# Kernel tuning notes

Measured on AMD Instinct MI355X. Metric: run time of the kernel, lower is better.

Reference implementation:

```python
import jax, jax.numpy as jnp
from jax import lax
import numpy as np

N_MTF = 41

def _gaussian2d(N, std):
    t = np.arange(-(N - 1) / 2, (N + 1) / 2)
    t1, t2 = np.meshgrid(t, t)
    return np.exp(-0.5 * (t1 / std) ** 2) * np.exp(-0.5 * (t2 / std) ** 2)

def _kaiser2d(N, beta):
    t = np.arange(-(N - 1) / 2, (N + 1) / 2) / np.double(N - 1)
    t1, t2 = np.meshgrid(t, t)
    t12 = np.sqrt(t1 * t1 + t2 * t2)
    w1 = np.kaiser(N, beta)
    w = np.interp(t12, t, w1)
    w[t12 > t[-1]] = 0
    w[t12 < t[0]] = 0
    return w

def _fir_filter_wind(Hd, w):
    hd = np.rot90(np.fft.fftshift(np.rot90(Hd, 2)), 2)
    h = np.fft.fftshift(np.fft.ifft2(hd))
    h = np.rot90(h, 2)
    return h * w

def gen_mtf_kernels(ratio, nbands):
    GNyq = np.asarray([0.34, 0.32, 0.3, 0.22], dtype='float32')[:nbands]  # QB sensor
    h = np.zeros((nbands, N_MTF, N_MTF), dtype='float32')
    fcut = 1.0 / ratio
    for ii in range(nbands):
        alpha = np.sqrt(((N_MTF - 1) * (fcut / 2)) ** 2 / (-2 * np.log(GNyq[ii])))
        H = _gaussian2d(N_MTF, alpha)
        Hd = H / np.max(H)
        w = _kaiser2d(N_MTF, 0.5)
        h[ii] = np.real(_fir_filter_wind(Hd, w)).astype('float32')
    return h

def gen_interp23_kernel():
    cdf23 = 2.0 * np.array([0.5, 0.305334091185, 0.0, -0.072698593239, 0.0,
                            0.021809577942, 0.0, -0.005192756653, 0.0,
                            0.000807762146, 0.0, -6.0081482e-05])
    d = cdf23[::-1]
    return np.concatenate([d[:-1], cdf23]).astype('float32')  # 23 taps

_DN = ('NCHW', 'OIHW', 'NCHW')

def _sep_filter_circular(img, k):
    # img: (bs, c, H, W); k: (K,) separable kernel, circular padding per torch F.pad('circular')
    bs, c, H, W = img.shape
    P = (k.shape[0] - 1) // 2
    f = img.reshape(bs * c, 1, H, W)
    f = jnp.pad(f, ((0, 0), (0, 0), (0, 0), (P, P)), mode='wrap')
    f = lax.conv_general_dilated(f, k.reshape(1, 1, 1, -1), (1, 1), 'VALID', dimension_numbers=_DN)
    f = jnp.pad(f, ((0, 0), (0, 0), (P, P), (0, 0)), mode='wrap')
    f = lax.conv_general_dilated(f, k.reshape(1, 1, -1, 1), (1, 1), 'VALID', dimension_numbers=_DN)
    return f.reshape(bs, c, H, W)

def interp23tap(x, kernel, num_upsamples):
    cur = x
    for k in range(num_upsamples):
        bs, c, h, w = cur.shape
        up = jnp.zeros((bs, c, 2 * h, 2 * w), cur.dtype)
        if k == 0:
            up = up.at[..., 1::2, 1::2].set(cur)
        else:
            up = up.at[..., ::2, ::2].set(cur)
        cur = _sep_filter_circular(up, kernel)
    return cur

def setup_inputs() -> dict:
    key = jax.random.key(0)
    bs, nbands, H, W = 4, 4, 1024, 1024
    ratio = 4
    x = jax.random.normal(key, (bs, nbands, H, W), dtype=jnp.float32)
    mtf_kernels = jnp.asarray(gen_mtf_kernels(ratio, nbands))          # (nbands, 41, 41)
    interp_kernel = jnp.asarray(gen_interp23_kernel())                  # (23,)
    pan_weights = jnp.full((nbands,), 1.0 / nbands, dtype=jnp.float32)  # 'mean' pan weights
    return {"x": x, "mtf_kernels": mtf_kernels, "interp_kernel": interp_kernel,
            "pan_weights": pan_weights, "ratio": ratio}

def reference(x, mtf_kernels, interp_kernel, pan_weights, ratio):
    # Simulated PAN: spectral weighting of HR bands
    pan = jnp.einsum('bchw,c->bhw', x, pan_weights)[:, None]  # (bs,1,H,W)
    # MTF blur: depthwise 41x41 conv with replicate padding
    nbands = x.shape[1]
    pad = mtf_kernels.shape[-1] // 2
    xp = jnp.pad(x, ((0, 0), (0, 0), (pad, pad), (pad, pad)), mode='edge')
    blurred = lax.conv_general_dilated(xp, mtf_kernels[:, None], (1, 1), 'VALID',
                                       dimension_numbers=_DN, feature_group_count=nbands)
    # Downsample: avgpool with kernel=stride=ratio
    bs, c, H, W = blurred.shape
    lrms = blurred.reshape(bs, c, H // ratio, ratio, W // ratio, ratio).mean(axis=(3, 5))
    # Upsample back via 23-tap polynomial interpolation (ratio = 2**num_upsamples)
    num_ups = int(ratio).bit_length() - 1
    ms_up = interp23tap(lrms, interp_kernel, num_ups)
    return pan, lrms, ms_up
```

## Files before the change

kernel.cpp:

```cpp
#include <hip/hip_runtime.h>

#define PAN_SZ  4194304
#define LRMS_OFF 4194304
#define MS_OFF  5242880

__global__ __launch_bounds__(256) void build_keff_kernel(
    const float* __restrict__ mtf, float* __restrict__ keff) {
  int e = blockIdx.x * 256 + threadIdx.x;
  if (e >= 4 * 44 * 44) return;
  int c = e / 1936;
  int rem = e - c * 1936;
  int p = rem / 44;
  int q = rem - p * 44;
  float s = 0.f;
  for (int di = 0; di < 4; ++di) {
    int u = p - di;
    if (u < 0 || u > 40) continue;
    for (int dj = 0; dj < 4; ++dj) {
      int v = q - dj;
      if (v < 0 || v > 40) continue;
      s += mtf[(c * 41 + u) * 41 + v];
    }
  }
  keff[e] = s * 0.0625f;
}

__global__ __launch_bounds__(256) void pan_kernel(
    const float* __restrict__ x, const float* __restrict__ w,
    float* __restrict__ pan) {
  int g = blockIdx.x * 256 + threadIdx.x;
  int b = g >> 18;
  int e = g & 262143;
  const float4* x4 = (const float4*)x;
  float w0 = w[0], w1 = w[1], w2 = w[2], w3 = w[3];
  float4 a0 = x4[(size_t)(b * 4 + 0) * 262144 + e];
  float4 a1 = x4[(size_t)(b * 4 + 1) * 262144 + e];
  float4 a2 = x4[(size_t)(b * 4 + 2) * 262144 + e];
  float4 a3 = x4[(size_t)(b * 4 + 3) * 262144 + e];
  float4 o;
  o.x = a0.x * w0 + a1.x * w1 + a2.x * w2 + a3.x * w3;
  o.y = a0.y * w0 + a1.y * w1 + a2.y * w2 + a3.y * w3;
  o.z = a0.z * w0 + a1.z * w1 + a2.z * w2 + a3.z * w3;
  o.w = a0.w * w0 + a1.w * w1 + a2.w * w2 + a3.w * w3;
  ((float4*)pan)[g] = o;
}

__global__ __launch_bounds__(256) void lrms_kernel(
    const float* __restrict__ x, const float* __restrict__ keff,
    float* __restrict__ lrms) {
  int img = blockIdx.y;
  int ch  = img & 3;
  int i0  = blockIdx.x * 8;
  int oc  = threadIdx.x;

  const float* ximg = x + (size_t)img * 1048576;
  const float* Kc   = keff + ch * 1936;

  float acc[8] = {0.f, 0.f, 0.f, 0.f, 0.f, 0.f, 0.f, 0.f};
  int c4base = oc - 5;
  bool interior = (oc >= 5) && (oc <= 250);

  float4 va[11], vb[11];

  auto loadrow = [&](int tt, float4* v) {
    int gy = 4 * i0 - 20 + tt;
    gy = gy < 0 ? 0 : (gy > 1023 ? 1023 : gy);
    const float4* row4 = (const float4*)(ximg + (size_t)gy * 1024);
    if (interior) {
      #pragma unroll
      for (int a = 0; a < 11; ++a) v[a] = row4[c4base + a];
    } else {
      const float* rowf = (const float*)row4;
      #pragma unroll
      for (int a = 0; a < 11; ++a) {
        int c4 = c4base + a;
        if ((unsigned)c4 <= 255u) {
          v[a] = row4[c4];
        } else {
          float4 t;
          t.x = rowf[min(max(4 * c4 + 0, 0), 1023)];
          t.y = rowf[min(max(4 * c4 + 1, 0), 1023)];
          t.z = rowf[min(max(4 * c4 + 2, 0), 1023)];
          t.w = rowf[min(max(4 * c4 + 3, 0), 1023)];
          v[a] = t;
        }
      }
    }
  };

  auto compute = [&](int tt, const float4* v) {
    #pragma unroll
    for (int r = 0; r < 8; ++r) {
      int p = tt - 4 * r;
      if ((unsigned)p < 44u) {
        const float* Kr = Kc + __builtin_amdgcn_readfirstlane(p * 44);
        float s = acc[r];
        #pragma unroll
        for (int a = 0; a < 11; ++a) {
          s += v[a].x * Kr[4 * a + 0] + v[a].y * Kr[4 * a + 1] +
               v[a].z * Kr[4 * a + 2] + v[a].w * Kr[4 * a + 3];
        }
        acc[r] = s;
      }
    }
  };

  loadrow(0, va);
  for (int it = 0; it < 36; ++it) {
    int tt = 2 * it;
    loadrow(tt + 1, vb);
    compute(tt, va);
    if (tt + 2 < 72) loadrow(tt + 2, va);
    compute(tt + 1, vb);
  }

  #pragma unroll
  for (int r = 0; r < 8; ++r)
    lrms[((size_t)img * 256 + i0 + r) * 256 + oc] = acc[r];
}

__global__ __launch_bounds__(256) void interp_kernel(
    const float* __restrict__ lrms, const float* __restrict__ ik,
    float* __restrict__ ms) {
  __shared__ float lr[32][33];
  __shared__ float t1[32][44];
  __shared__ float s1[43][44];
  __shared__ float t2[43][64];
  __shared__ float k2[12];

  int img = blockIdx.z;
  int bx = blockIdx.x, by = blockIdx.y;
  int tid = threadIdx.x;

  if (tid < 12) k2[tid] = ik[2 * tid];

  const float* L = lrms + (size_t)img * 65536;
  int ybase = by * 16 - 8, xbase = bx * 16 - 8;
  for (int e = tid; e < 32 * 32; e += 256) {
    int yy = e >> 5, xx = e & 31;
    int gy = (ybase + yy) & 255;
    int gx = (xbase + xx) & 255;
    lr[yy][xx] = L[gy * 256 + gx];
  }
  __syncthreads();

  for (int e = tid; e < 32 * 43; e += 256) {
    int yy = e / 43, cc = e - yy * 43;
    float val;
    if ((cc & 1) == 0) {
      val = lr[yy][(cc >> 1) + 5];
    } else {
      int base = (cc - 5) >> 1;
      float s = 0.f;
      #pragma unroll
      for (int t = 0; t < 12; ++t) s += k2[t] * lr[yy][base + 2 + t];
      val = s;
    }
    t1[yy][cc] = val;
  }
  __syncthreads();

  for (int e = tid; e < 43 * 43; e += 256) {
    int rr = e / 43, cc = e - rr * 43;
    float val;
    if ((rr & 1) == 0) {
      val = t1[(rr >> 1) + 5][cc];
    } else {
      int base = (rr - 5) >> 1;
      float s = 0.f;
      #pragma unroll
      for (int t = 0; t < 12; ++t) s += k2[t] * t1[base + 2 + t][cc];
      val = s;
    }
    s1[rr][cc] = val;
  }
  __syncthreads();

  for (int e = tid; e < 43 * 64; e += 256) {
    int rr = e >> 6, mm = e & 63;
    float val;
    if ((mm & 1) == 0) {
      val = s1[rr][(mm >> 1) + 5];
    } else {
      int base = (mm - 1) >> 1;
      float s = 0.f;
      #pragma unroll
      for (int t = 0; t < 12; ++t) s += k2[t] * s1[rr][base + t];
      val = s;
    }
    t2[rr][mm] = val;
  }
  __syncthreads();

  float* O = ms + (size_t)img * 1048576 + (size_t)(by * 64) * 1024 + bx * 64;
  for (int e = tid; e < 64 * 64; e += 256) {
    int nn = e >> 6, mm = e & 63;
    float val;
    if ((nn & 1) == 0) {
      val = t2[(nn >> 1) + 5][mm];
    } else {
      int base = (nn - 1) >> 1;
      float s = 0.f;
      #pragma unroll
      for (int t = 0; t < 12; ++t) s += k2[t] * t2[base + t][mm];
      val = s;
    }
    O[(size_t)nn * 1024 + mm] = val;
  }
}

extern "C" void kernel_launch(void* const* d_in, const int* in_sizes, int n_in,
                              void* d_out, int out_size, void* d_ws, size_t ws_size,
                              hipStream_t stream) {
  const float* x   = (const float*)d_in[0];
  const float* mtf = (const float*)d_in[1];
  const float* ik  = (const float*)d_in[2];
  const float* pw  = (const float*)d_in[3];
  float* out = (float*)d_out;
  float* keff = (float*)d_ws;

  build_keff_kernel<<<31, 256, 0, stream>>>(mtf, keff);
  pan_kernel<<<4096, 256, 0, stream>>>(x, pw, out);
  lrms_kernel<<<dim3(32, 16), 256, 0, stream>>>(x, keff, out + LRMS_OFF);
  interp_kernel<<<dim3(16, 16, 16), 256, 0, stream>>>(out + LRMS_OFF, ik, out + MS_OFF);
}
```

Measured before the change: 341.5 us.

## Collapse two-stage interp into 4-phase polyphase filters; halve lrms rows per block

The two cascaded 2x upsampling passes become one 4x polyphase separable filter. Its composed coefficients G are precomputed by a small kernel, so interp needs two shared-memory passes instead of four. The lrms kernel now computes 4 output rows per block with a grid twice as large, giving more blocks for occupancy. It also splits the per-row accumulator into float4 lanes to shorten the dependency chains. In exchange, each block rereads more overlapping input rows, and the composed-filter algebra must exactly match the cascaded reference.

```diff
diff --git a/kernel.cpp b/kernel.cpp
--- a/kernel.cpp
+++ b/kernel.cpp
@@ -1,6 +1,5 @@
 #include <hip/hip_runtime.h>
 
-#define PAN_SZ  4194304
 #define LRMS_OFF 4194304
 #define MS_OFF  5242880
 
@@ -23,6 +22,38 @@
     }
   }
   keff[e] = s * 0.0625f;
+}
+
+__global__ void build_gcoef_kernel(const float* __restrict__ ik,
+                                   float* __restrict__ G) {
+  int tid = threadIdx.x;
+  if (tid >= 68) return;
+  int d = tid / 17, oi = tid % 17, o = oi - 8;
+  float k2[12];
+  #pragma unroll
+  for (int t = 0; t < 12; ++t) k2[t] = ik[2 * t];
+  float g = 0.f;
+  if (d == 0) {
+    int t = o + 6;
+    if (t >= 0 && t < 12) g = k2[t];
+  } else if (d == 2) {
+    g = (o == 0) ? 1.f : 0.f;
+  } else if (d == 1) {
+    int t = 2 * (o + 3);
+    if (t >= 0 && t <= 10) g += k2[t];
+    for (int t1 = 1; t1 < 12; t1 += 2) {
+      int r = o + 6 - (t1 - 5) / 2;
+      if (r >= 0 && r < 12) g += k2[t1] * k2[r];
+    }
+  } else {
+    int t = 2 * o + 5;
+    if (t >= 1 && t <= 11) g += k2[t];
+    for (int t0 = 0; t0 <= 10; t0 += 2) {
+      int r = o + 8 - t0 / 2;
+      if (r >= 0 && r < 12) g += k2[t0] * k2[r];
+    }
+  }
+  G[d * 17 + oi] = g;
 }
 
 __global__ __launch_bounds__(256) void pan_kernel(
@@ -50,16 +81,18 @@
     float* __restrict__ lrms) {
   int img = blockIdx.y;
   int ch  = img & 3;
-  int i0  = blockIdx.x * 8;
+  int i0  = blockIdx.x * 4;
   int oc  = threadIdx.x;
 
   const float* ximg = x + (size_t)img * 1048576;
   const float* Kc   = keff + ch * 1936;
 
-  float acc[8] = {0.f, 0.f, 0.f, 0.f, 0.f, 0.f, 0.f, 0.f};
+  float4 acc[4];
+  #pragma unroll
+  for (int r = 0; r < 4; ++r) acc[r] = make_float4(0.f, 0.f, 0.f, 0.f);
+
   int c4base = oc - 5;
   bool interior = (oc >= 5) && (oc <= 250);
-
   float4 va[11], vb[11];
 
   auto loadrow = [&](int tt, float4* v) {
@@ -90,15 +123,17 @@
 
   auto compute = [&](int tt, const float4* v) {
     #pragma unroll
-    for (int r = 0; r < 8; ++r) {
+    for (int r = 0; r < 4; ++r) {
       int p = tt - 4 * r;
       if ((unsigned)p < 44u) {
         const float* Kr = Kc + __builtin_amdgcn_readfirstlane(p * 44);
-        float s = acc[r];
+        float4 s = acc[r];
         #pragma unroll
         for (int a = 0; a < 11; ++a) {
-          s += v[a].x * Kr[4 * a + 0] + v[a].y * Kr[4 * a + 1] +
-               v[a].z * Kr[4 * a + 2] + v[a].w * Kr[4 * a + 3];
+          s.x += v[a].x * Kr[4 * a + 0];
+          s.y += v[a].y * Kr[4 * a + 1];
+          s.z += v[a].z * Kr[4 * a + 2];
+          s.w += v[a].w * Kr[4 * a + 3];
         }
         acc[r] = s;
       }
@@ -106,106 +141,76 @@
   };
 
   loadrow(0, va);
-  for (int it = 0; it < 36; ++it) {
+  for (int it = 0; it < 28; ++it) {
     int tt = 2 * it;
     loadrow(tt + 1, vb);
     compute(tt, va);
-    if (tt + 2 < 72) loadrow(tt + 2, va);
+    if (tt + 2 < 56) loadrow(tt + 2, va);
     compute(tt + 1, vb);
   }
 
   #pragma unroll
-  for (int r = 0; r < 8; ++r)
-    lrms[((size_t)img * 256 + i0 + r) * 256 + oc] = acc[r];
+  for (int r = 0; r < 4; ++r) {
+    float s = acc[r].x + acc[r].y + acc[r].z + acc[r].w;
+    lrms[((size_t)img * 256 + i0 + r) * 256 + oc] = s;
+  }
 }
 
 __global__ __launch_bounds__(256) void interp_kernel(
-    const float* __restrict__ lrms, const float* __restrict__ ik,
+    const float* __restrict__ lrms, const float* __restrict__ G,
     float* __restrict__ ms) {
-  __shared__ float lr[32][33];
-  __shared__ float t1[32][44];
-  __shared__ float s1[43][44];
-  __shared__ float t2[43][64];
-  __shared__ float k2[12];
+  __shared__ float lr[32][48];
+  __shared__ float H[32][68];
+  __shared__ float Gs[4][17];
 
   int img = blockIdx.z;
   int bx = blockIdx.x, by = blockIdx.y;
   int tid = threadIdx.x;
 
-  if (tid < 12) k2[tid] = ik[2 * tid];
+  if (tid < 68) Gs[tid / 17][tid % 17] = G[tid];
 
   const float* L = lrms + (size_t)img * 65536;
   int ybase = by * 16 - 8, xbase = bx * 16 - 8;
-  for (int e = tid; e < 32 * 32; e += 256) {
+  for (int e = tid; e < 1024; e += 256) {
     int yy = e >> 5, xx = e & 31;
-    int gy = (ybase + yy) & 255;
-    int gx = (xbase + xx) & 255;
-    lr[yy][xx] = L[gy * 256 + gx];
+    lr[yy][xx] = L[((ybase + yy) & 255) * 256 + ((xbase + xx) & 255)];
   }
   __syncthreads();
 
-  for (int e = tid; e < 32 * 43; e += 256) {
-    int yy = e / 43, cc = e - yy * 43;
-    float val;
-    if ((cc & 1) == 0) {
-      val = lr[yy][(cc >> 1) + 5];
-    } else {
-      int base = (cc - 5) >> 1;
-      float s = 0.f;
-      #pragma unroll
-      for (int t = 0; t < 12; ++t) s += k2[t] * lr[yy][base + 2 + t];
-      val = s;
-    }
-    t1[yy][cc] = val;
+  for (int u = tid; u < 512; u += 256) {
+    int r = u >> 4, j = u & 15;
+    float t[17];
+    #pragma unroll
+    for (int o = 0; o < 17; ++o) t[o] = lr[r][j + o];
+    float h0 = 0.f, h1 = 0.f, h3 = 0.f;
+    #pragma unroll
+    for (int o = 2; o <= 13; ++o) h0 += Gs[0][o] * t[o];
+    #pragma unroll
+    for (int o = 0; o < 17; ++o) h1 += Gs[1][o] * t[o];
+    #pragma unroll
+    for (int o = 0; o < 17; ++o) h3 += Gs[3][o] * t[o];
+    float4 hv = make_float4(h0, h1, t[8], h3);
+    *(float4*)(&H[r][4 * j]) = hv;
   }
   __syncthreads();
 
-  for (int e = tid; e < 43 * 43; e += 256) {
-    int rr = e / 43, cc = e - rr * 43;
-    float val;
-    if ((rr & 1) == 0) {
-      val = t1[(rr >> 1) + 5][cc];
-    } else {
-      int base = (rr - 5) >> 1;
-      float s = 0.f;
-      #pragma unroll
-      for (int t = 0; t < 12; ++t) s += k2[t] * t1[base + 2 + t][cc];
-      val = s;
-    }
-    s1[rr][cc] = val;
-  }
-  __syncthreads();
-
-  for (int e = tid; e < 43 * 64; e += 256) {
-    int rr = e >> 6, mm = e & 63;
-    float val;
-    if ((mm & 1) == 0) {
-      val = s1[rr][(mm >> 1) + 5];
-    } else {
-      int base = (mm - 1) >> 1;
-      float s = 0.f;
-      #pragma unroll
-      for (int t = 0; t < 12; ++t) s += k2[t] * s1[rr][base + t];
-      val = s;
-    }
-    t2[rr][mm] = val;
-  }
-  __syncthreads();
-
   float* O = ms + (size_t)img * 1048576 + (size_t)(by * 64) * 1024 + bx * 64;
-  for (int e = tid; e < 64 * 64; e += 256) {
-    int nn = e >> 6, mm = e & 63;
-    float val;
-    if ((nn & 1) == 0) {
-      val = t2[(nn >> 1) + 5][mm];
-    } else {
-      int base = (nn - 1) >> 1;
-      float s = 0.f;
-      #pragma unroll
-      for (int t = 0; t < 12; ++t) s += k2[t] * t2[base + t][mm];
-      val = s;
-    }
-    O[(size_t)nn * 1024 + mm] = val;
+  for (int u = tid; u < 1024; u += 256) {
+    int il = u >> 6, X = u & 63;
+    float t[17];
+    #pragma unroll
+    for (int o = 0; o < 17; ++o) t[o] = H[il + o][X];
+    float v0 = 0.f, v1 = 0.f, v3 = 0.f;
+    #pragma unroll
+    for (int o = 2; o <= 13; ++o) v0 += Gs[0][o] * t[o];
+    #pragma unroll
+    for (int o = 0; o < 17; ++o) v1 += Gs[1][o] * t[o];
+    #pragma unroll
+    for (int o = 0; o < 17; ++o) v3 += Gs[3][o] * t[o];
+    O[(size_t)(4 * il + 0) * 1024 + X] = v0;
+    O[(size_t)(4 * il + 1) * 1024 + X] = v1;
+    O[(size_t)(4 * il + 2) * 1024 + X] = t[8];
+    O[(size_t)(4 * il + 3) * 1024 + X] = v3;
   }
 }
 
@@ -218,9 +223,11 @@
   const float* pw  = (const float*)d_in[3];
   float* out = (float*)d_out;
   float* keff = (float*)d_ws;
+  float* G    = keff + 7744;
 
   build_keff_kernel<<<31, 256, 0, stream>>>(mtf, keff);
+  build_gcoef_kernel<<<1, 128, 0, stream>>>(ik, G);
   pan_kernel<<<4096, 256, 0, stream>>>(x, pw, out);
-  lrms_kernel<<<dim3(32, 16), 256, 0, stream>>>(x, keff, out + LRMS_OFF);
-  interp_kernel<<<dim3(16, 16, 16), 256, 0, stream>>>(out + LRMS_OFF, ik, out + MS_OFF);
-}
+  lrms_kernel<<<dim3(64, 16), 256, 0, stream>>>(x, keff, out + LRMS_OFF);
+  interp_kernel<<<dim3(16, 16, 16), 256, 0, stream>>>(out + LRMS_OFF, G, out + MS_OFF);
+}
```

Result: faster. 330.2 us (-3.3%).
